# Performance work log

Measured on AMD Instinct MI355X. Metric: run time of the kernel, lower is better.

Reference implementation:

```python
import jax, jax.numpy as jnp
import numpy as np

EPS_LN = 1e-5
EPS_NORM = 1e-12


def _bilinear_matrix(in_size, out_size):
    # align_corners=True bilinear interpolation as a dense (out,in) matrix
    pos = np.arange(out_size) * (in_size - 1) / (out_size - 1)
    lo = np.floor(pos).astype(np.int64)
    hi = np.minimum(lo + 1, in_size - 1)
    frac = (pos - lo).astype(np.float32)
    M = np.zeros((out_size, in_size), np.float32)
    M[np.arange(out_size), lo] += 1.0 - frac
    M[np.arange(out_size), hi] += frac
    return jnp.asarray(M)

_M20 = _bilinear_matrix(7, 20)  # [20,7]


def _upsample(x):
    # bilinear 7x7 -> 20x20, align_corners=True: separable matmuls
    return jnp.einsum('ih,jw,nchw->ncij', _M20, _M20, x)


def _conv2d(x, w, b, stride, pad):
    out = jax.lax.conv_general_dilated(
        x, w, window_strides=(stride, stride),
        padding=[(pad, pad), (pad, pad)],
        dimension_numbers=('NCHW', 'OIHW', 'NCHW'))
    return out + b[None, :, None, None]


def _crn(x, t, ln_w, ln_b, w_t, b_t, w_s, b_s, w_m, b_m, w_l, b_l, acc_w, acc_b):
    # LayerNorm over last two dims [7,7] with elementwise affine
    mu = x.mean(axis=(-2, -1), keepdims=True)
    var = x.var(axis=(-2, -1), keepdims=True)
    xn = (x - mu) * jax.lax.rsqrt(var + EPS_LN) * ln_w + ln_b
    up = _upsample(xn)                      # [N,512,20,20]
    xs = _conv2d(up, w_s, b_s, 3, 1)        # [N,32,7,7]
    xm = _conv2d(up, w_m, b_m, 5, 9)        # [N,32,7,7]
    xl = _conv2d(up, w_l, b_l, 2, 1)        # [N,20,7,7]
    tu = _upsample(t)
    tc = _conv2d(tu, w_t, b_t, 2, 0)        # [N,16,7,7]
    cat = jnp.concatenate([xs, xm, xl, tc], axis=1)  # [N,100,7,7]
    return _conv2d(cat, acc_w, acc_b, 1, 0)          # [N,1,7,7]


def setup_inputs() -> dict:
    key = jax.random.key(0)
    ks = jax.random.split(key, 16)
    N, C, K = 512, 512, 64
    centroids = jax.random.uniform(ks[0], (K, C), dtype=jnp.float32)
    return {
        'x': jax.random.normal(ks[1], (N, C, 7, 7), dtype=jnp.float32),
        't': jax.random.normal(ks[2], (N, C, 7, 7), dtype=jnp.float32),
        'centroids': centroids,
        'conv_w': 2.0 * 100.0 * centroids,
        'conv_b': -100.0 * jnp.linalg.norm(centroids, axis=1),
        'ln_w': jnp.ones((7, 7), jnp.float32),
        'ln_b': jnp.zeros((7, 7), jnp.float32),
        'w_t': jax.random.normal(ks[3], (16, 512, 8, 8), jnp.float32) * 0.02,
        'b_t': jax.random.normal(ks[4], (16,), jnp.float32) * 0.02,
        'w_s': jax.random.normal(ks[5], (32, 512, 3, 3), jnp.float32) * 0.02,
        'b_s': jax.random.normal(ks[6], (32,), jnp.float32) * 0.02,
        'w_m': jax.random.normal(ks[7], (32, 512, 7, 7), jnp.float32) * 0.02,
        'b_m': jax.random.normal(ks[8], (32,), jnp.float32) * 0.02,
        'w_l': jax.random.normal(ks[9], (20, 512, 9, 9), jnp.float32) * 0.02,
        'b_l': jax.random.normal(ks[10], (20,), jnp.float32) * 0.02,
        'acc_w': jax.random.normal(ks[11], (1, 100, 1, 1), jnp.float32) * 0.1,
        'acc_b': jax.random.normal(ks[12], (1,), jnp.float32) * 0.1,
    }


def reference(x, t, centroids, conv_w, conv_b, ln_w, ln_b,
              w_t, b_t, w_s, b_s, w_m, b_m, w_l, b_l, acc_w, acc_b):
    N, C = x.shape[:2]
    K = centroids.shape[0]
    S = x.shape[2] * x.shape[3]  # 49

    # CRN context weights [N,1,S]
    cw = _crn(x, t, ln_w, ln_b, w_t, b_t, w_s, b_s, w_m, b_m, w_l, b_l,
              acc_w, acc_b).reshape(N, 1, S)

    # descriptor-wise L2 normalization over channel dim (F.normalize p=2 dim=1)
    nrm = jnp.sqrt(jnp.sum(x * x, axis=1, keepdims=True))
    xn = x / jnp.maximum(nrm, EPS_NORM)
    xf = xn.reshape(N, C, S)                 # [N,C,S]

    # 1x1 conv == per-pixel matmul with conv_w [K,C]
    logits = jnp.einsum('kc,ncs->nks', conv_w, xf) + conv_b[None, :, None]
    sa = jax.nn.softmax(logits, axis=1)      # softmax over clusters

    w = sa * cw                              # reweighting mask [N,K,S]
    # matmul decomposition of sum_s w*(x - c): avoids (N,K,C,S) tensor
    vlad = (jnp.einsum('nks,ncs->nkc', w, xf)
            - centroids[None] * jnp.sum(w, axis=-1)[..., None])  # [N,K,C]

    # intra-normalize over C, flatten, global L2 normalize
    vn = jnp.sqrt(jnp.sum(vlad * vlad, axis=2, keepdims=True))
    vlad = vlad / jnp.maximum(vn, EPS_NORM)
    vlad = vlad.reshape(N, K * C)
    gn = jnp.sqrt(jnp.sum(vlad * vlad, axis=1, keepdims=True))
    return vlad / jnp.maximum(gn, EPS_NORM)
```

## Files before the change

kernel.cpp:

```cpp
#include <hip/hip_runtime.h>
#include <cstdint>
#include <cstddef>


#define N_   512
#define C_   512
#define S_   49
#define CS_  25088

#define OFF_WBS   0u
#define OFF_WBM   4608u
#define OFF_WBL   29696u
#define OFF_WBT   71168u
#define OFF_BETA  103936u
#define OFF_WT    103952u
#define OFF_PLTH  136720u
#define OFF_PLTL  939536u
#define OFF_QTH   1742352u
#define OFF_QTL   2545168u
#define OFF_PWTH  3347984u
#define OFF_PWTL  3364368u
#define OFF_PB    3380752u
#define OFF_PBP   3380816u
#define OFF_MUR   3405904u
#define OFF_XS    3668048u
#define OFF_WR    3668048u
#define OFF_CWP2  16513104u
#define OFF_WSUM  19724368u
#define OFF_CENTT 19757136u

typedef __attribute__((ext_vector_type(8))) short bf16x8;
typedef __attribute__((ext_vector_type(4))) float f32x4;

__device__ __forceinline__ float wave_sum64(float v) {
  #pragma unroll
  for (int off = 32; off; off >>= 1) v += __shfl_xor(v, off, 64);
  return v;
}

__device__ __forceinline__ void bsplit(float f, short& h, short& l) {
  unsigned u = __float_as_uint(f);
  h = (short)(u >> 16);
  float hf = __uint_as_float(u & 0xffff0000u);
  l = (short)(__float_as_uint(f - hf) >> 16);
}

__device__ __forceinline__ float m20val(int r, int p) {
  float pos = (float)(r * 6) / 19.0f;
  int lo = (int)floorf(pos);
  int hi = min(lo + 1, 6);
  float fr = pos - (float)lo;
  float v = 0.f;
  if (p == lo) v += 1.f - fr;
  if (p == hi) v += fr;
  return v;
}

__global__ void k_wbar(const float* __restrict__ w_s, const float* __restrict__ w_m,
                       const float* __restrict__ w_l, const float* __restrict__ w_t,
                       const float* __restrict__ accw, const float* __restrict__ accb,
                       const float* __restrict__ b_s, const float* __restrict__ b_m,
                       const float* __restrict__ b_l, const float* __restrict__ b_t,
                       float* __restrict__ wbs, float* __restrict__ wbm,
                       float* __restrict__ wbl, float* __restrict__ wbt,
                       float* __restrict__ beta) {
  int id = blockIdx.x * 256 + threadIdx.x;
  if (id == 0) {
    float b = accb[0];
    for (int o = 0; o < 32; ++o) b = fmaf(accw[o],      b_s[o], b);
    for (int o = 0; o < 32; ++o) b = fmaf(accw[32 + o], b_m[o], b);
    for (int o = 0; o < 20; ++o) b = fmaf(accw[64 + o], b_l[o], b);
    for (int o = 0; o < 16; ++o) b = fmaf(accw[84 + o], b_t[o], b);
    beta[0] = b;
  }
  if (id < 4608) {
    int c = id / 9, uv = id % 9;
    float a = 0.f;
    for (int o = 0; o < 32; ++o) a = fmaf(accw[o], w_s[(size_t)(o * 512 + c) * 9 + uv], a);
    wbs[id] = a;
  } else if (id < 29696) {
    int i2 = id - 4608; int c = i2 / 49, uv = i2 % 49;
    float a = 0.f;
    for (int o = 0; o < 32; ++o) a = fmaf(accw[32 + o], w_m[(size_t)(o * 512 + c) * 49 + uv], a);
    wbm[i2] = a;
  } else if (id < 71168) {
    int i2 = id - 29696; int c = i2 / 81, uv = i2 % 81;
    float a = 0.f;
    for (int o = 0; o < 20; ++o) a = fmaf(accw[64 + o], w_l[(size_t)(o * 512 + c) * 81 + uv], a);
    wbl[i2] = a;
  } else {
    int i2 = id - 71168; int c = i2 / 64, uv = i2 % 64;
    float a = 0.f;
    for (int o = 0; o < 16; ++o) a = fmaf(accw[84 + o], w_t[(size_t)(o * 512 + c) * 64 + uv], a);
    wbt[i2] = a;
  }
}

__global__ void k_wt(const float* __restrict__ convw, const float* __restrict__ cent,
                     float* __restrict__ wT, float* __restrict__ centT) {
  int id = blockIdx.x * 256 + threadIdx.x;
  int id2 = id & 32767;
  int k = id2 & 63, c = id2 >> 6;
  if (id < 32768) wT[id2] = convw[(size_t)k * 512 + c];
  else            centT[id2] = cent[(size_t)k * 512 + c];
}

__global__ void k_xs(const float* __restrict__ x, float* __restrict__ xs,
                     float* __restrict__ mur) {
  int idx = blockIdx.x * 256 + threadIdx.x;
  const float* p = x + (size_t)idx * 49;
  float s1 = 0.f, s2 = 0.f;
  #pragma unroll
  for (int s = 0; s < 49; ++s) { float v = p[s]; s1 += v; s2 = fmaf(v, v, s2); }
  float m = s1 * (1.f / 49.f);
  float var = s2 * (1.f / 49.f) - m * m;
  float r = 1.f / sqrtf(var + 1e-5f);
  float* o = xs + (size_t)idx * 49;
  #pragma unroll
  for (int s = 0; s < 49; ++s) o[s] = p[s] * r;
  mur[idx] = m * r;
}

__global__ void __launch_bounds__(512) k_buildP(
    const float* __restrict__ wbs, const float* __restrict__ wbm,
    const float* __restrict__ wbl, const float* __restrict__ wbt,
    const float* __restrict__ lnw, const float* __restrict__ lnb,
    short* __restrict__ plth, short* __restrict__ pltl,
    short* __restrict__ qth,  short* __restrict__ qtl,
    short* __restrict__ pwth, short* __restrict__ pwtl,
    float* __restrict__ pbp) {
  __shared__ float M[20][7];
  __shared__ float tP[49][50];
  __shared__ float tQ[49][50];
  int c = blockIdx.x;
  int tid = threadIdx.x;
  if (tid < 140) { int r = tid / 7, p = tid % 7; M[r][p] = m20val(r, p); }
  __syncthreads();

  const float* wbsr = wbs + c * 9;
  const float* wbmr = wbm + c * 49;
  const float* wblr = wbl + c * 81;
  const float* wbtr = wbt + c * 64;

  for (int e = tid; e < 2401; e += 512) {
    int s = e / 49, q = e % 49;
    int i = q / 7, j = q % 7, pp = s / 7, qq = s % 7;

    float sumP = 0.f;
    {
      float rv[3];
      #pragma unroll
      for (int v = 0; v < 3; ++v) { int col = j * 3 - 1 + v; rv[v] = ((unsigned)col < 20u) ? M[col][qq] : 0.f; }
      #pragma unroll
      for (int u = 0; u < 3; ++u) {
        int row = i * 3 - 1 + u; float ru = ((unsigned)row < 20u) ? M[row][pp] : 0.f;
        float a = wbsr[u * 3 + 0] * rv[0];
        a = fmaf(wbsr[u * 3 + 1], rv[1], a);
        a = fmaf(wbsr[u * 3 + 2], rv[2], a);
        sumP = fmaf(ru, a, sumP);
      }
    }
    {
      float rv[7];
      #pragma unroll
      for (int v = 0; v < 7; ++v) { int col = j * 5 - 9 + v; rv[v] = ((unsigned)col < 20u) ? M[col][qq] : 0.f; }
      #pragma unroll
      for (int u = 0; u < 7; ++u) {
        int row = i * 5 - 9 + u; float ru = ((unsigned)row < 20u) ? M[row][pp] : 0.f;
        float a = 0.f;
        #pragma unroll
        for (int v = 0; v < 7; ++v) a = fmaf(wbmr[u * 7 + v], rv[v], a);
        sumP = fmaf(ru, a, sumP);
      }
    }
    {
      float rv[9];
      #pragma unroll
      for (int v = 0; v < 9; ++v) { int col = j * 2 - 1 + v; rv[v] = ((unsigned)col < 20u) ? M[col][qq] : 0.f; }
      #pragma unroll
      for (int u = 0; u < 9; ++u) {
        int row = i * 2 - 1 + u; float ru = ((unsigned)row < 20u) ? M[row][pp] : 0.f;
        float a = 0.f;
        #pragma unroll
        for (int v = 0; v < 9; ++v) a = fmaf(wblr[u * 9 + v], rv[v], a);
        sumP = fmaf(ru, a, sumP);
      }
    }
    tP[s][q] = sumP;

    float sumQ = 0.f;
    {
      float rv[8];
      #pragma unroll
      for (int v = 0; v < 8; ++v) { int col = j * 2 + v; rv[v] = ((unsigned)col < 20u) ? M[col][qq] : 0.f; }
      #pragma unroll
      for (int u = 0; u < 8; ++u) {
        int row = i * 2 + u; float ru = ((unsigned)row < 20u) ? M[row][pp] : 0.f;
        float a = 0.f;
        #pragma unroll
        for (int v = 0; v < 8; ++v) a = fmaf(wbtr[u * 8 + v], rv[v], a);
        sumQ = fmaf(ru, a, sumQ);
      }
    }
    tQ[s][q] = sumQ;
  }
  __syncthreads();

  for (int e = tid; e < 2401; e += 512) {
    int q = e / 49, s = e % 49;
    float pv = tP[s][q];
    float qv = tQ[s][q];
    int k = c * 49 + s;
    int slab = k >> 8;
    int kc = (k & 255) >> 5;
    int kg = (k >> 3) & 3;
    int off = k & 7;
    int nf = q >> 4, l15 = q & 15;
    size_t oidx = (size_t)slab * 16384 + kc * 2048 + nf * 512
                + (size_t)(kg * 16 + l15) * 8 + off;
    short h, l;
    bsplit(lnw[s] * pv, h, l); plth[oidx] = h; pltl[oidx] = l;
    bsplit(qv, h, l);          qth[oidx]  = h; qtl[oidx]  = l;
  }

  if (tid < 49) {
    int q = tid;
    float pw = 0.f, pb = 0.f;
    #pragma unroll 7
    for (int s = 0; s < 49; ++s) {
      float p = tP[s][q];
      pw = fmaf(lnw[s], p, pw);
      pb = fmaf(lnb[s], p, pb);
    }
    short h, l; bsplit(-pw, h, l);
    pwth[q * 512 + c] = h;
    pwtl[q * 512 + c] = l;
    pbp[q * 512 + c] = pb;
  }
}

__global__ void k_pb(const float* __restrict__ pbp, float* __restrict__ PB) {
  int q = blockIdx.x, lane = threadIdx.x;
  float a = 0.f;
  for (int c = lane; c < 512; c += 64) a += pbp[q * 512 + c];
  a = wave_sum64(a);
  if (lane == 0) PB[q] = a;
}

template <int SA, int SB>
__device__ __forceinline__ void mf_chunk1(const float* __restrict__ A,
                                          const short* __restrict__ Bh,
                                          const short* __restrict__ Bl,
                                          int k, int mbase, int l15, int kg,
                                          f32x4 (&acc)[4]) {
  bf16x8 ah, al;
  {
    const float* ap = A + (size_t)(mbase + l15) * SA + k + kg * 8;
    float4 v0 = *reinterpret_cast<const float4*>(ap);
    float4 v1 = *reinterpret_cast<const float4*>(ap + 4);
    float f[8] = {v0.x, v0.y, v0.z, v0.w, v1.x, v1.y, v1.z, v1.w};
    #pragma unroll
    for (int jj = 0; jj < 8; ++jj) { short hh, ll; bsplit(f[jj], hh, ll); ah[jj] = hh; al[jj] = ll; }
  }
  #pragma unroll
  for (int nf = 0; nf < 4; ++nf) {
    size_t bo = (size_t)(nf * 16 + l15) * SB + k + kg * 8;
    bf16x8 bh = *reinterpret_cast<const bf16x8*>(Bh + bo);
    bf16x8 bl = *reinterpret_cast<const bf16x8*>(Bl + bo);
    acc[nf] = __builtin_amdgcn_mfma_f32_16x16x32_bf16(ah, bh, acc[nf], 0, 0, 0);
    acc[nf] = __builtin_amdgcn_mfma_f32_16x16x32_bf16(ah, bl, acc[nf], 0, 0, 0);
    acc[nf] = __builtin_amdgcn_mfma_f32_16x16x32_bf16(al, bh, acc[nf], 0, 0, 0);
  }
}

__global__ void __launch_bounds__(64) k_cwg(
    const float* __restrict__ xs, const float* __restrict__ tin,
    const float* __restrict__ mur,
    const short* __restrict__ plth, const short* __restrict__ pltl,
    const short* __restrict__ qth,  const short* __restrict__ qtl,
    const short* __restrict__ pwth, const short* __restrict__ pwtl,
    float* __restrict__ cwp2) {
  __shared__ float at[16 * 272];
  int wgid = (blockIdx.x & 7) * 392 + (blockIdx.x >> 3);
  int slab = wgid >> 5, mt = wgid & 31;
  int lane = threadIdx.x;
  int l15 = lane & 15, kg = lane >> 4;
  int mbase = mt * 16;
  int k0 = slab * 256;

  f32x4 acc[4];
  #pragma unroll
  for (int nf = 0; nf < 4; ++nf) acc[nf] = (f32x4){0.f, 0.f, 0.f, 0.f};

  #pragma unroll 1
  for (int ph = 0; ph < 2; ++ph) {
    const float* A  = ph ? tin : xs;
    const short* Bh = ph ? qth : plth;
    const short* Bl = ph ? qtl : pltl;
    const short* bhb = Bh + (size_t)slab * 16384 + lane * 8;
    const short* blb = Bl + (size_t)slab * 16384 + lane * 8;

    bf16x8 pbh[2][4], pbl[2][4];
    #pragma unroll
    for (int nf = 0; nf < 4; ++nf) {
      pbh[0][nf] = *reinterpret_cast<const bf16x8*>(bhb + nf * 512);
      pbl[0][nf] = *reinterpret_cast<const bf16x8*>(blb + nf * 512);
    }

    __syncthreads();
    #pragma unroll
    for (int i = 0; i < 16; ++i) {
      int idx4 = i * 64 + lane;
      int row = idx4 >> 6, col4 = idx4 & 63;
      float4 v = *reinterpret_cast<const float4*>(
          &A[(size_t)(mbase + row) * CS_ + k0 + col4 * 4]);
      *reinterpret_cast<float4*>(&at[row * 272 + col4 * 4]) = v;
    }
    __syncthreads();

    #pragma unroll
    for (int kc = 0; kc < 8; ++kc) {
      int cur = kc & 1, nxt = cur ^ 1;
      if (kc < 7) {
        #pragma unroll
        for (int nf = 0; nf < 4; ++nf) {
          pbh[nxt][nf] = *reinterpret_cast<const bf16x8*>(bhb + (kc + 1) * 2048 + nf * 512);
          pbl[nxt][nf] = *reinterpret_cast<const bf16x8*>(blb + (kc + 1) * 2048 + nf * 512);
        }
      }
      bf16x8 ah, al;
      {
        const float* ap = &at[l15 * 272 + kc * 32 + kg * 8];
        float4 v0 = *reinterpret_cast<const float4*>(ap);
        float4 v1 = *reinterpret_cast<const float4*>(ap + 4);
        float f[8] = {v0.x, v0.y, v0.z, v0.w, v1.x, v1.y, v1.z, v1.w};
        #pragma unroll
        for (int jj = 0; jj < 8; ++jj) { short hh, ll; bsplit(f[jj], hh, ll); ah[jj] = hh; al[jj] = ll; }
      }
      #pragma unroll
      for (int nf = 0; nf < 4; ++nf) {
        acc[nf] = __builtin_amdgcn_mfma_f32_16x16x32_bf16(ah, pbh[cur][nf], acc[nf], 0, 0, 0);
        acc[nf] = __builtin_amdgcn_mfma_f32_16x16x32_bf16(ah, pbl[cur][nf], acc[nf], 0, 0, 0);
        acc[nf] = __builtin_amdgcn_mfma_f32_16x16x32_bf16(al, pbh[cur][nf], acc[nf], 0, 0, 0);
      }
    }
  }
  if (slab < 16)
    mf_chunk1<512, 512>(mur, pwth, pwtl, slab * 32, mbase, l15, kg, acc);

  #pragma unroll
  for (int nf = 0; nf < 4; ++nf)
    #pragma unroll
    for (int r = 0; r < 4; ++r) {
      int row = mbase + kg * 4 + r;
      int col = nf * 16 + l15;
      cwp2[(size_t)slab * 32768 + (size_t)row * 64 + col] = acc[nf][r];
    }
}

__global__ void __launch_bounds__(256) k_logits(
    const float* __restrict__ x, const float* __restrict__ wT,
    const float* __restrict__ convb, const float* __restrict__ cwp2,
    const float* __restrict__ beta, const float* __restrict__ pb,
    float* __restrict__ wr, float* __restrict__ wsum) {
  __shared__ float part[4][64][49];
  __shared__ float sqp[4][49];
  __shared__ float cw4[4 * 49];
  __shared__ float mx4[4 * 49];
  __shared__ float sm4[4 * 49];
  int n = blockIdx.x;
  int tid = threadIdx.x;
  int wu = __builtin_amdgcn_readfirstlane((int)(threadIdx.x >> 6));
  int lane = tid & 63;
  int sl = min(lane, 48);
  float* pf = &part[0][0][0];

  if (tid < 196) {
    int s = tid % 49, g = tid / 49;
    int st = (g < 2) ? g * 25 : 50 + (g - 2) * 24;
    int cnt = (g < 2) ? 25 : 24;
    const float* cp = cwp2 + (size_t)st * 32768 + (size_t)n * 64 + s;
    float a = 0.f;
    for (int i = 0; i < cnt; ++i) a += cp[(size_t)i * 32768];
    cw4[g * 49 + s] = a;
  }

  float acc[64];
  #pragma unroll
  for (int k = 0; k < 64; ++k) acc[k] = 0.f;
  float ssq = 0.f;
  const float* xb = x + (size_t)n * CS_ + (size_t)wu * (128 * 49);
  const float* wb = wT + wu * (128 * 64);
  #pragma unroll 1
  for (int c = 0; c < 128; ++c) {
    float xv = xb[c * 49 + sl];
    ssq = fmaf(xv, xv, ssq);
    const float* wrow = wb + c * 64;
    #pragma unroll
    for (int k = 0; k < 64; ++k) acc[k] = fmaf(wrow[k], xv, acc[k]);
  }
  if (lane < 49) {
    sqp[wu][lane] = ssq;
    #pragma unroll
    for (int k = 0; k < 64; ++k) part[wu][k][lane] = acc[k];
  }
  __syncthreads();

  float lg[16];
  int sg = tid / 49, s_ = tid % 49;
  float rnv = 0.f;
  if (tid < 196) {
    float sumsq = sqp[0][s_] + sqp[1][s_] + sqp[2][s_] + sqp[3][s_];
    rnv = 1.f / fmaxf(sqrtf(sumsq), 1e-12f);
    float mloc = -1e30f;
    #pragma unroll
    for (int kk = 0; kk < 16; ++kk) {
      int kq = sg * 16 + kk;
      float a = part[0][kq][s_] + part[1][kq][s_] + part[2][kq][s_] + part[3][kq][s_];
      lg[kk] = fmaf(a, rnv, convb[kq]);
      mloc = fmaxf(mloc, lg[kk]);
    }
    mx4[sg * 49 + s_] = mloc;
  }
  __syncthreads();
  if (tid < 196) {
    float m0 = fmaxf(fmaxf(mx4[s_], mx4[49 + s_]), fmaxf(mx4[98 + s_], mx4[147 + s_]));
    float sloc = 0.f;
    #pragma unroll
    for (int kk = 0; kk < 16; ++kk) { lg[kk] = expf(lg[kk] - m0); sloc += lg[kk]; }
    sm4[sg * 49 + s_] = sloc;
  }
  __syncthreads();
  if (tid < 196) {
    float ssum = sm4[s_] + sm4[49 + s_] + sm4[98 + s_] + sm4[147 + s_];
    float cwv = cw4[s_] + cw4[49 + s_] + cw4[98 + s_] + cw4[147 + s_] + beta[0] + pb[s_];
    float inv = cwv / ssum;
    float wrs = inv * rnv;
    #pragma unroll
    for (int kk = 0; kk < 16; ++kk) {
      int kq = sg * 16 + kk;
      wr[((size_t)n * 64 + kq) * 64 + s_] = lg[kk] * wrs;
      pf[kq * 49 + s_] = lg[kk] * inv;
    }
  }
  __syncthreads();
  if (tid < 64) {
    float a = 0.f;
    #pragma unroll 7
    for (int s = 0; s < 49; ++s) a += pf[tid * 49 + s];
    wsum[n * 64 + tid] = a;
  }
}

__global__ void __launch_bounds__(512) k_vlad(
    const float* __restrict__ x, const float* __restrict__ wr,
    const float* __restrict__ wsum, const float* __restrict__ centT,
    float* __restrict__ out) {
  __shared__ float vallds[128 * 65];
  __shared__ float ssqp[8][64];
  __shared__ float scal[64];
  int n = blockIdx.x;
  int tid = threadIdx.x;
  int w = __builtin_amdgcn_readfirstlane((int)(threadIdx.x >> 6));
  int k = tid & 63;

  const float* wp = wr + (size_t)n * 4096 + k * 64;
  float wreg[49];
  #pragma unroll
  for (int s = 0; s < 49; ++s) wreg[s] = wp[s];
  float wsk = wsum[n * 64 + k];
  float ssq = 0.f;

  const float* xb = x + (size_t)n * CS_;
  float* ob = out + (size_t)n * 32768;

  for (int h = 0; h < 4; ++h) {
    int c0 = h * 128;
    #pragma unroll 1
    for (int i = 0; i < 16; ++i) {
      int cc = w * 16 + i;
      int c = c0 + cc;
      const float* xrow = xb + (size_t)c * 49;
      float d0 = 0.f, d1 = 0.f, d2 = 0.f, d3 = 0.f;
      #pragma unroll
      for (int s = 0; s < 48; s += 4) {
        d0 = fmaf(wreg[s],     xrow[s],     d0);
        d1 = fmaf(wreg[s + 1], xrow[s + 1], d1);
        d2 = fmaf(wreg[s + 2], xrow[s + 2], d2);
        d3 = fmaf(wreg[s + 3], xrow[s + 3], d3);
      }
      d0 = fmaf(wreg[48], xrow[48], d0);
      float v = (d0 + d1) + (d2 + d3);
      v = fmaf(-centT[c * 64 + k], wsk, v);
      vallds[cc * 65 + k] = v;
      ssq = fmaf(v, v, ssq);
    }
    __syncthreads();
    #pragma unroll 4
    for (int idx = tid; idx < 8192; idx += 512) {
      int kk = idx >> 7, cc = idx & 127;
      ob[(size_t)kk * 512 + c0 + cc] = vallds[cc * 65 + kk];
    }
    __syncthreads();
  }
  ssqp[w][k] = ssq;
  __syncthreads();
  if (tid < 64) {
    float v2 = 0.f;
    #pragma unroll
    for (int ww = 0; ww < 8; ++ww) v2 += ssqp[ww][tid];
    float vn = sqrtf(v2);
    float den = fmaxf(vn, 1e-12f);
    float cr = vn / den; cr *= cr;
    float g = wave_sum64(cr);
    scal[tid] = 1.f / (den * fmaxf(sqrtf(g), 1e-12f));
  }
  __syncthreads();
  #pragma unroll 8
  for (int idx = tid; idx < 32768; idx += 512)
    ob[idx] *= scal[idx >> 9];
}

extern "C" void kernel_launch(void* const* d_in, const int* in_sizes, int n_in,
                              void* d_out, int out_size, void* d_ws, size_t ws_size,
                              hipStream_t stream) {
  const float* x     = (const float*)d_in[0];
  const float* t     = (const float*)d_in[1];
  const float* cent  = (const float*)d_in[2];
  const float* convw = (const float*)d_in[3];
  const float* convb = (const float*)d_in[4];
  const float* lnw   = (const float*)d_in[5];
  const float* lnb   = (const float*)d_in[6];
  const float* w_t   = (const float*)d_in[7];
  const float* b_t   = (const float*)d_in[8];
  const float* w_s   = (const float*)d_in[9];
  const float* b_s   = (const float*)d_in[10];
  const float* w_m   = (const float*)d_in[11];
  const float* b_m   = (const float*)d_in[12];
  const float* w_l   = (const float*)d_in[13];
  const float* b_l   = (const float*)d_in[14];
  const float* accw  = (const float*)d_in[15];
  const float* accb  = (const float*)d_in[16];
  float* ws  = (float*)d_ws;
  float* out = (float*)d_out;

  float* wbs  = ws + OFF_WBS;
  float* wbm  = ws + OFF_WBM;
  float* wbl  = ws + OFF_WBL;
  float* wbt  = ws + OFF_WBT;
  float* beta = ws + OFF_BETA;
  float* wT   = ws + OFF_WT;
  short* plth = (short*)(ws + OFF_PLTH);
  short* pltl = (short*)(ws + OFF_PLTL);
  short* qth  = (short*)(ws + OFF_QTH);
  short* qtl  = (short*)(ws + OFF_QTL);
  short* pwth = (short*)(ws + OFF_PWTH);
  short* pwtl = (short*)(ws + OFF_PWTL);
  float* PB   = ws + OFF_PB;
  float* pbp  = ws + OFF_PBP;
  float* mur  = ws + OFF_MUR;
  float* xs   = ws + OFF_XS;
  float* cwp2 = ws + OFF_CWP2;
  float* wr   = ws + OFF_WR;
  float* wsumb = ws + OFF_WSUM;
  float* centT = ws + OFF_CENTT;

  k_wbar<<<dim3(406), dim3(256), 0, stream>>>(w_s, w_m, w_l, w_t, accw, accb,
                                              b_s, b_m, b_l, b_t,
                                              wbs, wbm, wbl, wbt, beta);
  k_wt<<<dim3(256), dim3(256), 0, stream>>>(convw, cent, wT, centT);
  k_xs<<<dim3(1024), dim3(256), 0, stream>>>(x, xs, mur);
  hipMemsetAsync(ws + OFF_PLTH, 0, (size_t)3244032 * 4, stream);
  k_buildP<<<dim3(512), dim3(512), 0, stream>>>(wbs, wbm, wbl, wbt, lnw, lnb,
                                                plth, pltl, qth, qtl,
                                                pwth, pwtl, pbp);
  k_pb<<<dim3(49), dim3(64), 0, stream>>>(pbp, PB);
  k_cwg<<<dim3(3136), dim3(64), 0, stream>>>(xs, t, mur, plth, pltl, qth, qtl,
                                             pwth, pwtl, cwp2);
  k_logits<<<dim3(512), dim3(256), 0, stream>>>(x, wT, convb, cwp2, beta, PB, wr, wsumb);
  k_vlad<<<dim3(512), dim3(512), 0, stream>>>(x, wr, wsumb, centT, out);
}
```

Before: 246.7 us.

## Compute VLAD aggregation with split-bf16 MFMA instead of scalar FMA dot products

Rewrites k_vlad so that each block stages 128 channels of x into LDS, padded from 49 to 64 spatial positions. The w×x products are then computed with 16x16x32 bf16 MFMA instructions, using a hi/lo bf16 split (three MFMAs per tile) to approximate fp32 accuracy. k_logits now zero-fills the padded columns 49..63 of wr so the K=64 reduction stays correct. Block size drops to 256 threads and the results are transposed through a padded LDS tile before the coalesced store. The aim is to replace per-thread scalar FMA loops and uncoalesced row reads with matrix-core work, at the cost of extra conversion instructions and a small accuracy risk from the split-bf16 scheme.

Result: faster. 232.4 us (-5.8%).

```diff
diff --git a/kernel.cpp b/kernel.cpp
--- a/kernel.cpp
+++ b/kernel.cpp
@@ -375,6 +375,11 @@
   int sl = min(lane, 48);
   float* pf = &part[0][0][0];
 
+  for (int e = tid; e < 960; e += 256) {
+    int kq = e / 15, p = e % 15;
+    wr[((size_t)n * 64 + kq) * 64 + 49 + p] = 0.f;
+  }
+
   if (tid < 196) {
     int s = tid % 49, g = tid / 49;
     int st = (g < 2) ? g * 25 : 50 + (g - 2) * 24;
@@ -452,63 +457,110 @@
   }
 }
 
-__global__ void __launch_bounds__(512) k_vlad(
+__global__ void __launch_bounds__(256) k_vlad(
     const float* __restrict__ x, const float* __restrict__ wr,
     const float* __restrict__ wsum, const float* __restrict__ centT,
     float* __restrict__ out) {
-  __shared__ float vallds[128 * 65];
-  __shared__ float ssqp[8][64];
+  __shared__ float xt[128 * 68];
+  __shared__ float vl[64 * 129];
+  __shared__ float sp[16][64];
   __shared__ float scal[64];
   int n = blockIdx.x;
   int tid = threadIdx.x;
-  int w = __builtin_amdgcn_readfirstlane((int)(threadIdx.x >> 6));
-  int k = tid & 63;
-
-  const float* wp = wr + (size_t)n * 4096 + k * 64;
-  float wreg[49];
-  #pragma unroll
-  for (int s = 0; s < 49; ++s) wreg[s] = wp[s];
-  float wsk = wsum[n * 64 + k];
-  float ssq = 0.f;
-
+  int w = tid >> 6, lane = tid & 63;
+  int l15 = lane & 15, kg = lane >> 4;
   const float* xb = x + (size_t)n * CS_;
+  const float* wrb = wr + (size_t)n * 4096;
+  const float* wsb = wsum + n * 64;
   float* ob = out + (size_t)n * 32768;
 
+  for (int e = tid; e < 1920; e += 256) {
+    int row = e / 15, col = 49 + e % 15;
+    xt[row * 68 + col] = 0.f;
+  }
+
+  float wsk[4];
+  #pragma unroll
+  for (int nf = 0; nf < 4; ++nf) wsk[nf] = wsb[nf * 16 + l15];
+  float ssqa[4] = {0.f, 0.f, 0.f, 0.f};
+
+  #pragma unroll 1
   for (int h = 0; h < 4; ++h) {
     int c0 = h * 128;
-    #pragma unroll 1
-    for (int i = 0; i < 16; ++i) {
-      int cc = w * 16 + i;
-      int c = c0 + cc;
-      const float* xrow = xb + (size_t)c * 49;
-      float d0 = 0.f, d1 = 0.f, d2 = 0.f, d3 = 0.f;
-      #pragma unroll
-      for (int s = 0; s < 48; s += 4) {
-        d0 = fmaf(wreg[s],     xrow[s],     d0);
-        d1 = fmaf(wreg[s + 1], xrow[s + 1], d1);
-        d2 = fmaf(wreg[s + 2], xrow[s + 2], d2);
-        d3 = fmaf(wreg[s + 3], xrow[s + 3], d3);
-      }
-      d0 = fmaf(wreg[48], xrow[48], d0);
-      float v = (d0 + d1) + (d2 + d3);
-      v = fmaf(-centT[c * 64 + k], wsk, v);
-      vallds[cc * 65 + k] = v;
-      ssq = fmaf(v, v, ssq);
-    }
+    __syncthreads();
+    for (int e = tid; e < 6272; e += 256) {
+      int row = e / 49, col = e % 49;
+      xt[row * 68 + col] = xb[(size_t)c0 * 49 + e];
+    }
+    __syncthreads();
+
+    f32x4 acc[2][4];
+    #pragma unroll
+    for (int mf = 0; mf < 2; ++mf)
+      #pragma unroll
+      for (int nf = 0; nf < 4; ++nf)
+        acc[mf][nf] = (f32x4){0.f, 0.f, 0.f, 0.f};
+
+    #pragma unroll
+    for (int kc = 0; kc < 2; ++kc) {
+      bf16x8 bh[4], bl[4];
+      #pragma unroll
+      for (int nf = 0; nf < 4; ++nf) {
+        const float* bp = wrb + (nf * 16 + l15) * 64 + kc * 32 + kg * 8;
+        float4 v0 = *reinterpret_cast<const float4*>(bp);
+        float4 v1 = *reinterpret_cast<const float4*>(bp + 4);
+        float f[8] = {v0.x, v0.y, v0.z, v0.w, v1.x, v1.y, v1.z, v1.w};
+        #pragma unroll
+        for (int jj = 0; jj < 8; ++jj) { short hh, ll; bsplit(f[jj], hh, ll); bh[nf][jj] = hh; bl[nf][jj] = ll; }
+      }
+      #pragma unroll
+      for (int mf = 0; mf < 2; ++mf) {
+        bf16x8 ah, al;
+        {
+          const float* ap = &xt[(w * 32 + mf * 16 + l15) * 68 + kc * 32 + kg * 8];
+          float4 v0 = *reinterpret_cast<const float4*>(ap);
+          float4 v1 = *reinterpret_cast<const float4*>(ap + 4);
+          float f[8] = {v0.x, v0.y, v0.z, v0.w, v1.x, v1.y, v1.z, v1.w};
+          #pragma unroll
+          for (int jj = 0; jj < 8; ++jj) { short hh, ll; bsplit(f[jj], hh, ll); ah[jj] = hh; al[jj] = ll; }
+        }
+        #pragma unroll
+        for (int nf = 0; nf < 4; ++nf) {
+          acc[mf][nf] = __builtin_amdgcn_mfma_f32_16x16x32_bf16(ah, bh[nf], acc[mf][nf], 0, 0, 0);
+          acc[mf][nf] = __builtin_amdgcn_mfma_f32_16x16x32_bf16(ah, bl[nf], acc[mf][nf], 0, 0, 0);
+          acc[mf][nf] = __builtin_amdgcn_mfma_f32_16x16x32_bf16(al, bh[nf], acc[mf][nf], 0, 0, 0);
+        }
+      }
+    }
+
+    #pragma unroll
+    for (int mf = 0; mf < 2; ++mf)
+      #pragma unroll
+      for (int nf = 0; nf < 4; ++nf)
+        #pragma unroll
+        for (int r = 0; r < 4; ++r) {
+          int cc = w * 32 + mf * 16 + kg * 4 + r;
+          int c = c0 + cc;
+          int k = nf * 16 + l15;
+          float v = fmaf(-centT[c * 64 + k], wsk[nf], acc[mf][nf][r]);
+          vl[k * 129 + cc] = v;
+          ssqa[nf] = fmaf(v, v, ssqa[nf]);
+        }
     __syncthreads();
     #pragma unroll 4
-    for (int idx = tid; idx < 8192; idx += 512) {
-      int kk = idx >> 7, cc = idx & 127;
-      ob[(size_t)kk * 512 + c0 + cc] = vallds[cc * 65 + kk];
-    }
-    __syncthreads();
-  }
-  ssqp[w][k] = ssq;
+    for (int e = tid; e < 8192; e += 256) {
+      int k = e >> 7, cc = e & 127;
+      ob[(size_t)k * 512 + c0 + cc] = vl[k * 129 + cc];
+    }
+  }
+
+  #pragma unroll
+  for (int nf = 0; nf < 4; ++nf) sp[w * 4 + kg][nf * 16 + l15] = ssqa[nf];
   __syncthreads();
   if (tid < 64) {
     float v2 = 0.f;
     #pragma unroll
-    for (int ww = 0; ww < 8; ++ww) v2 += ssqp[ww][tid];
+    for (int j = 0; j < 16; ++j) v2 += sp[j][tid];
     float vn = sqrtf(v2);
     float den = fmaxf(vn, 1e-12f);
     float cr = vn / den; cr *= cr;
@@ -517,7 +569,7 @@
   }
   __syncthreads();
   #pragma unroll 8
-  for (int idx = tid; idx < 32768; idx += 512)
+  for (int idx = tid; idx < 32768; idx += 256)
     ob[idx] *= scal[idx >> 9];
 }
 
@@ -578,5 +630,5 @@
   k_cwg<<<dim3(3136), dim3(64), 0, stream>>>(xs, t, mur, plth, pltl, qth, qtl,
                                              pwth, pwtl, cwp2);
   k_logits<<<dim3(512), dim3(256), 0, stream>>>(x, wT, convb, cwp2, beta, PB, wr, wsumb);
-  k_vlad<<<dim3(512), dim3(512), 0, stream>>>(x, wr, wsumb, centT, out);
-}
+  k_vlad<<<dim3(512), dim3(256), 0, stream>>>(x, wr, wsumb, centT, out);
+}
```
